# Optimization experiments

Measured on AMD Instinct MI355X. Metric: run time of the kernel, lower is better.

The kernel has to match this reference:

```python
import jax, jax.numpy as jnp
import numpy as np

B = 32        # events per batch
NP = 1024     # hits per event (in_hits)
K = 30        # kNN neighbors (includes self, as in PyG knn)
D_IN = 7      # hit feature dim (hardcoded SegmentationNet(7, ...))
OUT = 2       # out_channels


def _edge_conv(x, W1, b1, s, t, W2, b2, k):
    """DynamicEdgeConv: x [B,n,d] -> [B,n,64].
    kNN in feature space, edge MLP on [x_i, x_j - x_i], max-aggregate.
    BN (eval mode) folded into per-channel scale s and shift t."""
    sq = jnp.sum(x * x, axis=-1)                           # [B,n]
    d2 = sq[:, :, None] + sq[:, None, :] - 2.0 * jnp.einsum('bnd,bmd->bnm', x, x)
    _, idx = jax.lax.top_k(-d2, k)                         # [B,n,k] nearest (self included)
    xj = jax.vmap(lambda xb, ib: xb[ib])(x, idx)           # [B,n,k,d] gather neighbors
    xi = jnp.broadcast_to(x[:, :, None, :], xj.shape)
    e = jnp.concatenate([xi, xj - xi], axis=-1)            # [B,n,k,2d]
    h = jax.nn.relu((e @ W1 + b1) * s + t)                 # Linear + BN(eval) + ReLU
    h = h @ W2 + b2                                        # plain last layer (PyG MLP)
    return jnp.max(h, axis=2)                              # max aggregation over k


def setup_inputs() -> dict:
    key = jax.random.key(0)
    ks = jax.random.split(key, 40)
    def lin(k, fi, fo):
        return jax.random.normal(k, (fi, fo), jnp.float32) / np.float32(np.sqrt(fi))
    def vec(k, n, scale=0.1):
        return jax.random.normal(k, (n,), jnp.float32) * np.float32(scale)
    inp = {}
    inp['pos'] = jax.random.normal(ks[0], (B * NP, D_IN), jnp.float32)
    inp['batch'] = jnp.repeat(jnp.arange(B, dtype=jnp.int32), NP)
    inp['batch_size'] = B
    # conv1 edge MLP: [14,64] + BN + ReLU, [64,64]
    inp['c1_W1'] = lin(ks[1], 2 * D_IN, 64); inp['c1_b1'] = vec(ks[2], 64)
    inp['c1_s'] = 1.0 + vec(ks[3], 64); inp['c1_t'] = vec(ks[4], 64)
    inp['c1_W2'] = lin(ks[5], 64, 64); inp['c1_b2'] = vec(ks[6], 64)
    # conv2/conv3: [128,64] + BN + ReLU, [64,64]
    inp['c2_W1'] = lin(ks[7], 128, 64); inp['c2_b1'] = vec(ks[8], 64)
    inp['c2_s'] = 1.0 + vec(ks[9], 64); inp['c2_t'] = vec(ks[10], 64)
    inp['c2_W2'] = lin(ks[11], 64, 64); inp['c2_b2'] = vec(ks[12], 64)
    inp['c3_W1'] = lin(ks[13], 128, 64); inp['c3_b1'] = vec(ks[14], 64)
    inp['c3_s'] = 1.0 + vec(ks[15], 64); inp['c3_t'] = vec(ks[16], 64)
    inp['c3_W2'] = lin(ks[17], 64, 64); inp['c3_b2'] = vec(ks[18], 64)
    # segmentation head MLP [192,1024,256,128,OUT], norm=None, eval (dropout off)
    inp['h_W1'] = lin(ks[19], 192, 1024); inp['h_b1'] = vec(ks[20], 1024)
    inp['h_W2'] = lin(ks[21], 1024, 256); inp['h_b2'] = vec(ks[22], 256)
    inp['h_W3'] = lin(ks[23], 256, 128); inp['h_b3'] = vec(ks[24], 128)
    inp['h_W4'] = lin(ks[25], 128, OUT); inp['h_b4'] = vec(ks[26], OUT)
    # wrapper MLP: Linear(NP*OUT, 100), ReLU, Linear(100, OUT)
    inp['m_W1'] = lin(ks[27], NP * OUT, 100); inp['m_b1'] = vec(ks[28], 100)
    inp['m_W2'] = lin(ks[29], 100, OUT); inp['m_b2'] = vec(ks[30], OUT)
    return inp


def reference(pos, batch, batch_size,
              c1_W1, c1_b1, c1_s, c1_t, c1_W2, c1_b2,
              c2_W1, c2_b1, c2_s, c2_t, c2_W2, c2_b2,
              c3_W1, c3_b1, c3_s, c3_t, c3_W2, c3_b2,
              h_W1, h_b1, h_W2, h_b2, h_W3, h_b3, h_W4, h_b4,
              m_W1, m_b1, m_W2, m_b2):
    n = pos.shape[0] // batch_size
    x = pos.reshape(batch_size, n, -1)          # uniform contiguous graphs per `batch`
    x1 = _edge_conv(x, c1_W1, c1_b1, c1_s, c1_t, c1_W2, c1_b2, K)
    x2 = _edge_conv(x1, c2_W1, c2_b1, c2_s, c2_t, c2_W2, c2_b2, K)
    x3 = _edge_conv(x2, c3_W1, c3_b1, c3_s, c3_t, c3_W2, c3_b2, K)
    h = jnp.concatenate([x1, x2, x3], axis=-1)  # [B,n,192]
    h = jax.nn.relu(h @ h_W1 + h_b1)
    h = jax.nn.relu(h @ h_W2 + h_b2)
    h = jax.nn.relu(h @ h_W3 + h_b3)
    h = h @ h_W4 + h_b4
    seg = jax.nn.log_softmax(h, axis=-1)        # per-node log-probs [B,n,OUT]
    flat = seg.reshape(batch_size, -1)          # [B, n*OUT]
    y = jax.nn.relu(flat @ m_W1 + m_b1) @ m_W2 + m_b2
    return jax.nn.log_softmax(y, axis=-1)       # [B, OUT]
```

## Files before the change

kernel.cpp:

```cpp
#include <hip/hip_runtime.h>
#include <math.h>

#define NPB   1024
#define NB    32
#define NTOT  (NPB * NB)
#define KNN_K 30
#define QB    16
#define DSTR  1028
#define FINF  __builtin_inff()

typedef __attribute__((ext_vector_type(8))) short bf16x8;
typedef __attribute__((ext_vector_type(4))) float f32x4;
typedef unsigned short ushort_t;

__device__ inline ushort_t f2bf(float f) {
  unsigned u = __builtin_bit_cast(unsigned, f);
  u += 0x7FFFu + ((u >> 16) & 1u);
  return (ushort_t)(u >> 16);
}
__device__ inline float bf2f(ushort_t h) {
  return __builtin_bit_cast(float, (unsigned)h << 16);
}
__device__ inline unsigned packkey(float d, int col) {
  unsigned u = __builtin_bit_cast(unsigned, d);
  u ^= ((unsigned)((int)u >> 31) | 0x80000000u);
  return (u & 0xFFFFFC00u) | (unsigned)col;
}

__device__ __forceinline__ void select_row_packed(const unsigned* row, int jbase,
                                                  int* out, unsigned* cb, int lane) {
  unsigned u[16];
  #pragma unroll
  for (int i = 0; i < 16; ++i) u[i] = row[lane + (i << 6)];

  unsigned m = u[0];
  #pragma unroll
  for (int i = 1; i < 16; ++i) m = min(m, u[i]);
  #pragma unroll
  for (int k = 2; k <= 64; k <<= 1) {
    #pragma unroll
    for (int jj = k >> 1; jj >= 1; jj >>= 1) {
      const unsigned o = (unsigned)__shfl_xor((int)m, jj);
      const bool up    = ((lane & k) == 0);
      const bool lower = ((lane & jj) == 0);
      m = (lower == up) ? min(m, o) : max(m, o);
    }
  }
  const unsigned T = (unsigned)__shfl((int)m, 29);

  unsigned mask16 = 0; int cnt = 0;
  #pragma unroll
  for (int i = 0; i < 16; ++i) {
    const bool sv = (u[i] <= T);
    mask16 |= (sv ? 1u : 0u) << i;
    cnt += sv;
  }
  int sc = cnt;
  #pragma unroll
  for (int o = 1; o < 64; o <<= 1) {
    const int v = __shfl_up(sc, o);
    if (lane >= o) sc += v;
  }
  const int base = sc - cnt;
  const int tot  = __shfl(sc, 63);

  if (tot <= 128) {
    int p = base;
    #pragma unroll
    for (int i = 0; i < 16; ++i) {
      if ((mask16 >> i) & 1u) cb[p++] = u[i];
    }
    for (int q = tot + lane; q < 128; q += 64) cb[q] = 0xFFFFFFFFu;
    unsigned r0 = cb[lane];
    unsigned r1 = cb[lane + 64];
    #pragma unroll
    for (int k = 2; k <= 128; k <<= 1) {
      #pragma unroll
      for (int jj = k >> 1; jj >= 1; jj >>= 1) {
        if (jj == 64) {
          const unsigned lo = min(r0, r1), hi = max(r0, r1);
          r0 = lo; r1 = hi;
        } else {
          const unsigned o0 = (unsigned)__shfl_xor((int)r0, jj);
          const unsigned o1 = (unsigned)__shfl_xor((int)r1, jj);
          const bool lower = ((lane & jj) == 0);
          const bool up0 = ((lane & k) == 0);
          const bool up1 = (((lane + 64) & k) == 0);
          r0 = (lower == up0) ? min(r0, o0) : max(r0, o0);
          r1 = (lower == up1) ? min(r1, o1) : max(r1, o1);
        }
      }
    }
    if (lane < KNN_K) out[lane] = jbase + (int)(r0 & 1023u);
  } else {
    unsigned pk[16];
    #pragma unroll
    for (int i = 0; i < 16; ++i) pk[i] = u[i];
    #pragma unroll 1
    for (int k = 0; k < KNN_K; ++k) {
      unsigned best = pk[0];
      #pragma unroll
      for (int i = 1; i < 16; ++i) best = min(best, pk[i]);
      #pragma unroll
      for (int o = 32; o > 0; o >>= 1)
        best = min(best, (unsigned)__shfl_xor((int)best, o));
      if (lane == 0) out[k] = jbase + (int)(best & 1023u);
      #pragma unroll
      for (int i = 0; i < 16; ++i) if (pk[i] == best) pk[i] = 0xFFFFFFFFu;
    }
  }
}

__global__ __launch_bounds__(512)
void knn64_kernel(const ushort_t* __restrict__ X, int lda,
                  const float* __restrict__ sq, int* __restrict__ idx) {
  __shared__ unsigned d2l[QB * DSTR];
  __shared__ float sqa[QB];
  __shared__ unsigned cbuf[8][128];
  const int tid = threadIdx.x;
  const int wave = tid >> 6, lane = tid & 63;
  const int g = lane >> 4, r16 = lane & 15;
  const int nbase = blockIdx.y * NPB;
  const int q0 = blockIdx.x * QB;
  if (tid < QB) sqa[tid] = sq[nbase + q0 + tid];
  __syncthreads();

  const int n0 = wave * 128;
  bf16x8 a0[2];
  #pragma unroll
  for (int ks = 0; ks < 2; ++ks)
    a0[ks] = *(const bf16x8*)(X + (size_t)(nbase + q0 + r16) * lda + ks * 32 + g * 8);

  #pragma unroll
  for (int nt = 0; nt < 8; ++nt) {
    const int col = n0 + nt * 16 + r16;
    f32x4 acc0 = (f32x4)(0.f);
    #pragma unroll
    for (int ks = 0; ks < 2; ++ks) {
      const bf16x8 b = *(const bf16x8*)(X + (size_t)(nbase + col) * lda + ks * 32 + g * 8);
      acc0 = __builtin_amdgcn_mfma_f32_16x16x32_bf16(a0[ks], b, acc0, 0, 0, 0);
    }
    const float sb = sq[nbase + col];
    #pragma unroll
    for (int r = 0; r < 4; ++r) {
      const int row0 = g * 4 + r;
      d2l[row0 * DSTR + col] = packkey(sqa[row0] + sb - 2.f * acc0[r], col);
    }
  }
  __syncthreads();

  #pragma unroll 1
  for (int rr = 0; rr < 2; ++rr) {
    const int row = wave * 2 + rr;
    select_row_packed(&d2l[row * DSTR], nbase,
                      idx + (size_t)(nbase + q0 + row) * KNN_K, cbuf[wave], lane);
  }
}

__global__ __launch_bounds__(512)
void knn7_kernel(const float* __restrict__ pos,
                 const float* __restrict__ sq, int* __restrict__ idx) {
  __shared__ unsigned d2l[QB * DSTR];
  __shared__ float Xq[QB][8];
  __shared__ float sqa[QB];
  __shared__ unsigned cbuf[8][128];
  const int tid = threadIdx.x;
  const int wave = tid >> 6, lane = tid & 63;
  const int nbase = blockIdx.y * NPB;
  const int q0 = blockIdx.x * QB;
  if (tid < QB * 8) {
    const int row = tid >> 3, d = tid & 7;
    Xq[row][d] = (d < 7) ? pos[(size_t)(nbase + q0 + row) * 7 + d] : 0.f;
  }
  if (tid >= 256 && tid < 256 + QB) sqa[tid - 256] = sq[nbase + q0 + tid - 256];
  __syncthreads();

  const int c0 = wave * 128 + lane;
  float xc0[7], xc1[7];
  #pragma unroll
  for (int d = 0; d < 7; ++d) {
    xc0[d] = pos[(size_t)(nbase + c0) * 7 + d];
    xc1[d] = pos[(size_t)(nbase + c0 + 64) * 7 + d];
  }
  const float sb0 = sq[nbase + c0], sb1 = sq[nbase + c0 + 64];
  #pragma unroll 1
  for (int row = 0; row < QB; ++row) {
    float q[7];
    #pragma unroll
    for (int d = 0; d < 7; ++d) q[d] = Xq[row][d];
    float d0 = 0.f, d1 = 0.f;
    #pragma unroll
    for (int d = 0; d < 7; ++d) { d0 += q[d] * xc0[d]; d1 += q[d] * xc1[d]; }
    const float sa = sqa[row];
    d2l[row * DSTR + c0]      = packkey(sa + sb0 - 2.f * d0, c0);
    d2l[row * DSTR + c0 + 64] = packkey(sa + sb1 - 2.f * d1, c0 + 64);
  }
  __syncthreads();

  #pragma unroll 1
  for (int rr = 0; rr < 2; ++rr) {
    const int row = wave * 2 + rr;
    select_row_packed(&d2l[row * DSTR], nbase,
                      idx + (size_t)(nbase + q0 + row) * KNN_K, cbuf[wave], lane);
  }
}

template<int D>
__global__ __launch_bounds__(256)
void sq_kernel(const float* __restrict__ x, int lda, float* __restrict__ sq) {
  const int wave = threadIdx.x >> 6, c = threadIdx.x & 63;
  const int nb = blockIdx.x * 16 + wave * 4;
  #pragma unroll
  for (int i = 0; i < 4; ++i) {
    const float xv = (c < D) ? x[(size_t)(nb + i) * lda + c] : 0.f;
    float p = xv * xv;
    #pragma unroll
    for (int o = 32; o > 0; o >>= 1) p += __shfl_down(p, o);
    if (c == 0) sq[nb + i] = p;
  }
}
__global__ __launch_bounds__(256)
void sqbf_kernel(const ushort_t* __restrict__ x, int lda, float* __restrict__ sq) {
  const int wave = threadIdx.x >> 6, c = threadIdx.x & 63;
  const int nb = blockIdx.x * 16 + wave * 4;
  #pragma unroll
  for (int i = 0; i < 4; ++i) {
    const float xv = bf2f(x[(size_t)(nb + i) * lda + c]);
    float p = xv * xv;
    #pragma unroll
    for (int o = 32; o > 0; o >>= 1) p += __shfl_down(p, o);
    if (c == 0) sq[nb + i] = p;
  }
}

__global__ __launch_bounds__(256)
void wprep_kernel(const float* __restrict__ W1, const float* __restrict__ b1,
                  const float* __restrict__ s, const float* __restrict__ t,
                  int D, ushort_t* __restrict__ BTc, float* __restrict__ biasc) {
  const int i = blockIdx.x * 256 + threadIdx.x;
  if (i >= 128 * 64) return;
  const int n = i >> 6, k = i & 63;
  float v = 0.f;
  if (k < D) {
    if (n < 64) v = (W1[k * 64 + n] - W1[(D + k) * 64 + n]) * s[n];
    else        v = W1[(D + k) * 64 + (n - 64)] * s[n - 64];
  }
  BTc[i] = f2bf(v);
  if (k == 0) biasc[n] = (n < 64) ? (b1[n] * s[n] + t[n]) : 0.f;
}

__global__ __launch_bounds__(256)
void pospad_kernel(const float* __restrict__ pos, ushort_t* __restrict__ xpad) {
  const int i = blockIdx.x * 256 + threadIdx.x;
  const int node = i >> 6, k = i & 63;
  xpad[i] = f2bf(k < 7 ? pos[(size_t)node * 7 + k] : 0.f);
}

__global__ __launch_bounds__(256)
void wcvt_kernel(const float* __restrict__ W, ushort_t* __restrict__ BT,
                 int K, int N) {
  const int i = blockIdx.x * 256 + threadIdx.x;
  if (i >= N * K) return;
  const int n = i / K, k = i % K;
  BT[i] = f2bf(W[(size_t)k * N + n]);
}

__global__ __launch_bounds__(256)
void edge_mfma_kernel(const ushort_t* __restrict__ av,
                      const int* __restrict__ idx,
                      const ushort_t* __restrict__ W2T, const float* __restrict__ b2,
                      ushort_t* __restrict__ xbf) {
  const int lane = threadIdx.x & 63;
  const int wave = threadIdx.x >> 6;
  const int g = lane >> 4, r16 = lane & 15;
  const int node0 = blockIdx.x * 16 + wave * 4;

  bf16x8 bf[2][4];
  #pragma unroll
  for (int ks = 0; ks < 2; ++ks)
    #pragma unroll
    for (int nt = 0; nt < 4; ++nt)
      bf[ks][nt] = *(const bf16x8*)(W2T + (nt * 16 + r16) * 64 + ks * 32 + g * 8);

  const float b2c = b2[lane];

  #pragma unroll 1
  for (int nn = 0; nn < 4; ++nn) {
    const int node = node0 + nn;
    float asf[2][8];
    {
      const ushort_t* ar = av + (size_t)node * 128;
      #pragma unroll
      for (int ks = 0; ks < 2; ++ks) {
        union { uint4 v; ushort_t s[8]; } u;
        u.v = *(const uint4*)(ar + ks * 32 + g * 8);
        #pragma unroll
        for (int i = 0; i < 8; ++i) asf[ks][i] = bf2f(u.s[i]);
      }
    }
    const int j0 = idx[(size_t)node * KNN_K + r16];
    const int e1 = 16 + r16;
    const int j1 = idx[(size_t)node * KNN_K + (e1 < KNN_K ? e1 : KNN_K - 1)];

    f32x4 acc[2][4];
    #pragma unroll
    for (int mt = 0; mt < 2; ++mt)
      #pragma unroll
      for (int nt = 0; nt < 4; ++nt) acc[mt][nt] = (f32x4)(0.f);

    #pragma unroll
    for (int mt = 0; mt < 2; ++mt) {
      const int j = mt ? j1 : j0;
      const ushort_t* vr = av + (size_t)j * 128 + 64;
      #pragma unroll
      for (int ks = 0; ks < 2; ++ks) {
        union { uint4 v; ushort_t s[8]; } u;
        u.v = *(const uint4*)(vr + ks * 32 + g * 8);
        bf16x8 af;
        #pragma unroll
        for (int i = 0; i < 8; ++i) {
          const float hh = fmaxf(asf[ks][i] + bf2f(u.s[i]), 0.f);
          af[i] = (short)f2bf(hh);
        }
        #pragma unroll
        for (int nt = 0; nt < 4; ++nt)
          acc[mt][nt] = __builtin_amdgcn_mfma_f32_16x16x32_bf16(af, bf[ks][nt], acc[mt][nt], 0, 0, 0);
      }
    }

    float cm[4];
    #pragma unroll
    for (int nt = 0; nt < 4; ++nt) {
      float m0 = fmaxf(fmaxf(acc[0][nt][0], acc[0][nt][1]), fmaxf(acc[0][nt][2], acc[0][nt][3]));
      float m1 = fmaxf(fmaxf(acc[1][nt][0], acc[1][nt][1]), fmaxf(acc[1][nt][2], acc[1][nt][3]));
      float m = fmaxf(m0, m1);
      m = fmaxf(m, __shfl_xor(m, 16));
      m = fmaxf(m, __shfl_xor(m, 32));
      cm[nt] = m;
    }
    const float v = (g == 0) ? cm[0] : (g == 1) ? cm[1] : (g == 2) ? cm[2] : cm[3];
    xbf[(size_t)node * 192 + lane] = f2bf(v + b2c);
  }
}

template<bool RELU, typename CT>
__global__ __launch_bounds__(256)
void gemm_bf16_kernel(const ushort_t* __restrict__ A, int lda,
                      const ushort_t* __restrict__ BT, int ldb,
                      const float* __restrict__ bias,
                      CT* __restrict__ C, int ldc, int K) {
  __shared__ ushort_t As[128 * 72];
  __shared__ ushort_t Bs[128 * 72];
  const int tid = threadIdx.x;
  const int lane = tid & 63;
  const int g = lane >> 4, r16 = lane & 15;
  const int wv = tid >> 6, wm = wv >> 1, wn = wv & 1;
  const int bm = blockIdx.x * 128, bn = blockIdx.y * 128;

  f32x4 acc[4][4];
  #pragma unroll
  for (int mt = 0; mt < 4; ++mt)
    #pragma unroll
    for (int nt = 0; nt < 4; ++nt) acc[mt][nt] = (f32x4)(0.f);

  const int srow = tid >> 1, scq = (tid & 1) * 32;
  for (int k0 = 0; k0 < K; k0 += 64) {
    const ushort_t* ap = A + (size_t)(bm + srow) * lda + k0 + scq;
    const ushort_t* bp = BT + (size_t)(bn + srow) * ldb + k0 + scq;
    uint4 av0 = *(const uint4*)(ap);      uint4 av1 = *(const uint4*)(ap + 8);
    uint4 av2 = *(const uint4*)(ap + 16); uint4 av3 = *(const uint4*)(ap + 24);
    uint4 bv0 = *(const uint4*)(bp);      uint4 bv1 = *(const uint4*)(bp + 8);
    uint4 bv2 = *(const uint4*)(bp + 16); uint4 bv3 = *(const uint4*)(bp + 24);
    __syncthreads();
    *(uint4*)(As + srow * 72 + scq +  0) = av0;
    *(uint4*)(As + srow * 72 + scq +  8) = av1;
    *(uint4*)(As + srow * 72 + scq + 16) = av2;
    *(uint4*)(As + srow * 72 + scq + 24) = av3;
    *(uint4*)(Bs + srow * 72 + scq +  0) = bv0;
    *(uint4*)(Bs + srow * 72 + scq +  8) = bv1;
    *(uint4*)(Bs + srow * 72 + scq + 16) = bv2;
    *(uint4*)(Bs + srow * 72 + scq + 24) = bv3;
    __syncthreads();
    #pragma unroll
    for (int ks = 0; ks < 2; ++ks) {
      bf16x8 a[4], b[4];
      #pragma unroll
      for (int mt = 0; mt < 4; ++mt)
        a[mt] = *(const bf16x8*)(As + (wm * 64 + mt * 16 + r16) * 72 + ks * 32 + g * 8);
      #pragma unroll
      for (int nt = 0; nt < 4; ++nt)
        b[nt] = *(const bf16x8*)(Bs + (wn * 64 + nt * 16 + r16) * 72 + ks * 32 + g * 8);
      #pragma unroll
      for (int mt = 0; mt < 4; ++mt)
        #pragma unroll
        for (int nt = 0; nt < 4; ++nt)
          acc[mt][nt] = __builtin_amdgcn_mfma_f32_16x16x32_bf16(a[mt], b[nt], acc[mt][nt], 0, 0, 0);
    }
  }

  #pragma unroll
  for (int nt = 0; nt < 4; ++nt) {
    const int col = bn + wn * 64 + nt * 16 + r16;
    const float bv = bias[col];
    #pragma unroll
    for (int mt = 0; mt < 4; ++mt) {
      #pragma unroll
      for (int r = 0; r < 4; ++r) {
        const int row = bm + wm * 64 + mt * 16 + g * 4 + r;
        float val = acc[mt][nt][r] + bv;
        if (RELU) val = fmaxf(val, 0.f);
        if constexpr (sizeof(CT) == 2) C[(size_t)row * ldc + col] = f2bf(val);
        else                           C[(size_t)row * ldc + col] = val;
      }
    }
  }
}

__global__ __launch_bounds__(256)
void g4_kernel(const ushort_t* __restrict__ h3, const float* __restrict__ W4,
               const float* __restrict__ b4, float* __restrict__ seg) {
  const int row = blockIdx.x * 4 + (threadIdx.x >> 6);
  const int lane = threadIdx.x & 63;
  const ushort_t* hr = h3 + (size_t)row * 128;
  float p0 = 0.f, p1 = 0.f;
  #pragma unroll
  for (int h = 0; h < 2; ++h) {
    const int r = lane + h * 64;
    const float hv = bf2f(hr[r]);
    p0 += hv * W4[r * 2 + 0];
    p1 += hv * W4[r * 2 + 1];
  }
  #pragma unroll
  for (int o = 32; o > 0; o >>= 1) { p0 += __shfl_down(p0, o); p1 += __shfl_down(p1, o); }
  if (lane == 0) {
    const float l0 = p0 + b4[0], l1 = p1 + b4[1];
    const float mx = fmaxf(l0, l1);
    const float lse = mx + logf(expf(l0 - mx) + expf(l1 - mx));
    seg[(size_t)row * 2 + 0] = l0 - lse;
    seg[(size_t)row * 2 + 1] = l1 - lse;
  }
}

__global__ __launch_bounds__(256)
void wrapper_kernel(const float* __restrict__ seg, const float* __restrict__ W1,
                    const float* __restrict__ b1, const float* __restrict__ W2,
                    const float* __restrict__ b2, float* __restrict__ out) {
  __shared__ float fl[NPB * 2];
  __shared__ float part[2][128];
  __shared__ float y1[100];
  __shared__ float l2[2];
  const int b = blockIdx.x, tid = threadIdx.x;
  for (int i = tid; i < NPB * 2; i += 256) fl[i] = seg[(size_t)b * NPB * 2 + i];
  __syncthreads();
  {
    const int c = tid & 127, p = tid >> 7;
    float acc = 0.f;
    if (c < 100) {
      const int r0 = p * (NPB);
      #pragma unroll 16
      for (int r = 0; r < NPB; ++r)
        acc += fl[r0 + r] * W1[(size_t)(r0 + r) * 100 + c];
    }
    part[p][c] = acc;
  }
  __syncthreads();
  if (tid < 100) {
    y1[tid] = fmaxf(part[0][tid] + part[1][tid] + b1[tid], 0.f);
  }
  __syncthreads();
  if (tid < 2) {
    float acc = b2[tid];
    for (int j = 0; j < 100; ++j) acc += y1[j] * W2[j * 2 + tid];
    l2[tid] = acc;
  }
  __syncthreads();
  if (tid == 0) {
    const float l0 = l2[0], l1 = l2[1];
    const float mx = fmaxf(l0, l1);
    const float lse = mx + logf(expf(l0 - mx) + expf(l1 - mx));
    out[b * 2 + 0] = l0 - lse;
    out[b * 2 + 1] = l1 - lse;
  }
}

extern "C" void kernel_launch(void* const* d_in, const int* in_sizes, int n_in,
                              void* d_out, int out_size, void* d_ws, size_t ws_size,
                              hipStream_t stream) {
  const float* pos   = (const float*)d_in[0];
  const float* c1_W1 = (const float*)d_in[3];
  const float* c1_b1 = (const float*)d_in[4];
  const float* c1_s  = (const float*)d_in[5];
  const float* c1_t  = (const float*)d_in[6];
  const float* c1_W2 = (const float*)d_in[7];
  const float* c1_b2 = (const float*)d_in[8];
  const float* c2_W1 = (const float*)d_in[9];
  const float* c2_b1 = (const float*)d_in[10];
  const float* c2_s  = (const float*)d_in[11];
  const float* c2_t  = (const float*)d_in[12];
  const float* c2_W2 = (const float*)d_in[13];
  const float* c2_b2 = (const float*)d_in[14];
  const float* c3_W1 = (const float*)d_in[15];
  const float* c3_b1 = (const float*)d_in[16];
  const float* c3_s  = (const float*)d_in[17];
  const float* c3_t  = (const float*)d_in[18];
  const float* c3_W2 = (const float*)d_in[19];
  const float* c3_b2 = (const float*)d_in[20];
  const float* h_W1  = (const float*)d_in[21];
  const float* h_b1  = (const float*)d_in[22];
  const float* h_W2  = (const float*)d_in[23];
  const float* h_b2  = (const float*)d_in[24];
  const float* h_W3  = (const float*)d_in[25];
  const float* h_b3  = (const float*)d_in[26];
  const float* h_W4  = (const float*)d_in[27];
  const float* h_b4  = (const float*)d_in[28];
  const float* m_W1  = (const float*)d_in[29];
  const float* m_b1  = (const float*)d_in[30];
  const float* m_W2  = (const float*)d_in[31];
  const float* m_b2  = (const float*)d_in[32];

  float* ws = (float*)d_ws;
  size_t off = 0;
  auto alloc = [&](size_t n) {
    float* p = ws + off;
    off += (n + 63) & ~(size_t)63;
    return p;
  };
  ushort_t* xbf   = (ushort_t*)alloc((size_t)NTOT * 96);
  int*      idx   = (int*)alloc((size_t)NTOT * KNN_K);
  ushort_t* avbuf = (ushort_t*)alloc((size_t)NTOT * 64);
  ushort_t* xpad  = (ushort_t*)alloc((size_t)NTOT * 32);
  float*    sqb   = alloc(NTOT);
  float*    seg   = alloc((size_t)NTOT * 2);
  ushort_t* BT1   = (ushort_t*)alloc(1024 * 192 / 2);
  ushort_t* BT2   = (ushort_t*)alloc(256 * 1024 / 2);
  ushort_t* BT3   = (ushort_t*)alloc(128 * 256 / 2);
  ushort_t* BTc1  = (ushort_t*)alloc(128 * 64 / 2);
  ushort_t* BTc2  = (ushort_t*)alloc(128 * 64 / 2);
  ushort_t* BTc3  = (ushort_t*)alloc(128 * 64 / 2);
  ushort_t* W2T1  = (ushort_t*)alloc(64 * 64 / 2);
  ushort_t* W2T2  = (ushort_t*)alloc(64 * 64 / 2);
  ushort_t* W2T3  = (ushort_t*)alloc(64 * 64 / 2);
  float*    bc1   = alloc(128);
  float*    bc2   = alloc(128);
  float*    bc3   = alloc(128);

  const size_t totf = ws_size / 4;
  const size_t avail = (totf > off + 1024) ? (totf - off - 1024) : 0;
  int CH = 1;
  while (CH < 256 && (size_t)(NTOT / CH) * 704 > avail) CH <<= 1;
  const int CR = NTOT / CH;
  ushort_t* h1 = (ushort_t*)(ws + off);
  ushort_t* h2 = h1 + (size_t)CR * 1024;
  ushort_t* h3 = h2 + (size_t)CR * 256;

  wcvt_kernel<<<(192 * 1024 + 255) / 256, 256, 0, stream>>>(h_W1, BT1, 192, 1024);
  wcvt_kernel<<<(1024 * 256 + 255) / 256, 256, 0, stream>>>(h_W2, BT2, 1024, 256);
  wcvt_kernel<<<(256 * 128 + 255) / 256, 256, 0, stream>>>(h_W3, BT3, 256, 128);
  wcvt_kernel<<<16, 256, 0, stream>>>(c1_W2, W2T1, 64, 64);
  wcvt_kernel<<<16, 256, 0, stream>>>(c2_W2, W2T2, 64, 64);
  wcvt_kernel<<<16, 256, 0, stream>>>(c3_W2, W2T3, 64, 64);
  wprep_kernel<<<32, 256, 0, stream>>>(c1_W1, c1_b1, c1_s, c1_t, 7,  BTc1, bc1);
  wprep_kernel<<<32, 256, 0, stream>>>(c2_W1, c2_b1, c2_s, c2_t, 64, BTc2, bc2);
  wprep_kernel<<<32, 256, 0, stream>>>(c3_W1, c3_b1, c3_s, c3_t, 64, BTc3, bc3);
  pospad_kernel<<<NTOT * 64 / 256, 256, 0, stream>>>(pos, xpad);

  auto run_av = [&](const ushort_t* A, int lda, const ushort_t* BTc, const float* bc) {
    gemm_bf16_kernel<false, ushort_t><<<dim3(NTOT / 128, 1), 256, 0, stream>>>(
        A, lda, BTc, 64, bc, avbuf, 128, 64);
  };

  sq_kernel<7><<<NTOT / 16, 256, 0, stream>>>(pos, 7, sqb);
  run_av(xpad, 64, BTc1, bc1);
  knn7_kernel<<<dim3(NPB / QB, NB), 512, 0, stream>>>(pos, sqb, idx);
  edge_mfma_kernel<<<NTOT / 16, 256, 0, stream>>>(avbuf, idx, W2T1, c1_b2, xbf + 0);

  sqbf_kernel<<<NTOT / 16, 256, 0, stream>>>(xbf + 0, 192, sqb);
  run_av(xbf + 0, 192, BTc2, bc2);
  knn64_kernel<<<dim3(NPB / QB, NB), 512, 0, stream>>>(xbf + 0, 192, sqb, idx);
  edge_mfma_kernel<<<NTOT / 16, 256, 0, stream>>>(avbuf, idx, W2T2, c2_b2, xbf + 64);

  sqbf_kernel<<<NTOT / 16, 256, 0, stream>>>(xbf + 64, 192, sqb);
  run_av(xbf + 64, 192, BTc3, bc3);
  knn64_kernel<<<dim3(NPB / QB, NB), 512, 0, stream>>>(xbf + 64, 192, sqb, idx);
  edge_mfma_kernel<<<NTOT / 16, 256, 0, stream>>>(avbuf, idx, W2T3, c3_b2, xbf + 128);

  for (int ch = 0; ch < CH; ++ch) {
    const ushort_t* Ax = xbf + (size_t)ch * CR * 192;
    gemm_bf16_kernel<true, ushort_t><<<dim3(CR / 128, 8), 256, 0, stream>>>(Ax, 192, BT1, 192, h_b1, h1, 1024, 192);
    gemm_bf16_kernel<true, ushort_t><<<dim3(CR / 128, 2), 256, 0, stream>>>(h1, 1024, BT2, 1024, h_b2, h2, 256, 1024);
    gemm_bf16_kernel<true, ushort_t><<<dim3(CR / 128, 1), 256, 0, stream>>>(h2, 256, BT3, 256, h_b3, h3, 128, 256);
    g4_kernel<<<CR / 4, 256, 0, stream>>>(h3, h_W4, h_b4, seg + (size_t)ch * CR * 2);
  }

  wrapper_kernel<<<NB, 256, 0, stream>>>(seg, m_W1, m_b1, m_W2, m_b2, (float*)d_out);
}
```

Baseline: 414.1 us.

## Halve kNN query block, reuse distance row as candidate buffer, add 64-wide sort path

Cuts the kNN query block from 16 to 8 rows, so each wave selects one row and each block uses about half the LDS. That raises occupancy and doubles the block count. The separate candidate buffer is dropped, and the already-loaded distance row is reused in place to compact survivors. A new fast path handles up to 64 candidates with a single-register bitonic sort, skipping the 128-wide sort. In the MFMA path, half of the 16 rows computed are wasted and masked out, and the query-row loads are clamped.

```diff
diff --git a/kernel.cpp b/kernel.cpp
--- a/kernel.cpp
+++ b/kernel.cpp
@@ -5,7 +5,7 @@
 #define NB    32
 #define NTOT  (NPB * NB)
 #define KNN_K 30
-#define QB    16
+#define QB    8
 #define DSTR  1028
 #define FINF  __builtin_inff()
 
@@ -27,8 +27,8 @@
   return (u & 0xFFFFFC00u) | (unsigned)col;
 }
 
-__device__ __forceinline__ void select_row_packed(const unsigned* row, int jbase,
-                                                  int* out, unsigned* cb, int lane) {
+__device__ __forceinline__ void select_row_packed(unsigned* row, int jbase,
+                                                  int* out, int lane) {
   unsigned u[16];
   #pragma unroll
   for (int i = 0; i < 16; ++i) u[i] = row[lane + (i << 6)];
@@ -63,8 +63,28 @@
   }
   const int base = sc - cnt;
   const int tot  = __shfl(sc, 63);
-
-  if (tot <= 128) {
+  unsigned* cb = row;
+
+  if (tot <= 64) {
+    int p = base;
+    #pragma unroll
+    for (int i = 0; i < 16; ++i) {
+      if ((mask16 >> i) & 1u) cb[p++] = u[i];
+    }
+    if (tot + lane < 64) cb[tot + lane] = 0xFFFFFFFFu;
+    unsigned r0 = cb[lane];
+    #pragma unroll
+    for (int k = 2; k <= 64; k <<= 1) {
+      #pragma unroll
+      for (int jj = k >> 1; jj >= 1; jj >>= 1) {
+        const unsigned o = (unsigned)__shfl_xor((int)r0, jj);
+        const bool up    = ((lane & k) == 0);
+        const bool lower = ((lane & jj) == 0);
+        r0 = (lower == up) ? min(r0, o) : max(r0, o);
+      }
+    }
+    if (lane < KNN_K) out[lane] = jbase + (int)(r0 & 1023u);
+  } else if (tot <= 128) {
     int p = base;
     #pragma unroll
     for (int i = 0; i < 16; ++i) {
@@ -116,7 +136,6 @@
                   const float* __restrict__ sq, int* __restrict__ idx) {
   __shared__ unsigned d2l[QB * DSTR];
   __shared__ float sqa[QB];
-  __shared__ unsigned cbuf[8][128];
   const int tid = threadIdx.x;
   const int wave = tid >> 6, lane = tid & 63;
   const int g = lane >> 4, r16 = lane & 15;
@@ -126,10 +145,11 @@
   __syncthreads();
 
   const int n0 = wave * 128;
+  const int qr = (r16 < QB) ? r16 : QB - 1;
   bf16x8 a0[2];
   #pragma unroll
   for (int ks = 0; ks < 2; ++ks)
-    a0[ks] = *(const bf16x8*)(X + (size_t)(nbase + q0 + r16) * lda + ks * 32 + g * 8);
+    a0[ks] = *(const bf16x8*)(X + (size_t)(nbase + q0 + qr) * lda + ks * 32 + g * 8);
 
   #pragma unroll
   for (int nt = 0; nt < 8; ++nt) {
@@ -144,17 +164,15 @@
     #pragma unroll
     for (int r = 0; r < 4; ++r) {
       const int row0 = g * 4 + r;
-      d2l[row0 * DSTR + col] = packkey(sqa[row0] + sb - 2.f * acc0[r], col);
-    }
-  }
-  __syncthreads();
-
-  #pragma unroll 1
-  for (int rr = 0; rr < 2; ++rr) {
-    const int row = wave * 2 + rr;
-    select_row_packed(&d2l[row * DSTR], nbase,
-                      idx + (size_t)(nbase + q0 + row) * KNN_K, cbuf[wave], lane);
-  }
+      if (row0 < QB)
+        d2l[row0 * DSTR + col] = packkey(sqa[row0] + sb - 2.f * acc0[r], col);
+    }
+  }
+  __syncthreads();
+
+  const int row = wave;
+  select_row_packed(&d2l[row * DSTR], nbase,
+                    idx + (size_t)(nbase + q0 + row) * KNN_K, lane);
 }
 
 __global__ __launch_bounds__(512)
@@ -163,7 +181,6 @@
   __shared__ unsigned d2l[QB * DSTR];
   __shared__ float Xq[QB][8];
   __shared__ float sqa[QB];
-  __shared__ unsigned cbuf[8][128];
   const int tid = threadIdx.x;
   const int wave = tid >> 6, lane = tid & 63;
   const int nbase = blockIdx.y * NPB;
@@ -172,7 +189,7 @@
     const int row = tid >> 3, d = tid & 7;
     Xq[row][d] = (d < 7) ? pos[(size_t)(nbase + q0 + row) * 7 + d] : 0.f;
   }
-  if (tid >= 256 && tid < 256 + QB) sqa[tid - 256] = sq[nbase + q0 + tid - 256];
+  if (tid >= 64 && tid < 64 + QB) sqa[tid - 64] = sq[nbase + q0 + tid - 64];
   __syncthreads();
 
   const int c0 = wave * 128 + lane;
@@ -183,7 +200,7 @@
     xc1[d] = pos[(size_t)(nbase + c0 + 64) * 7 + d];
   }
   const float sb0 = sq[nbase + c0], sb1 = sq[nbase + c0 + 64];
-  #pragma unroll 1
+  #pragma unroll
   for (int row = 0; row < QB; ++row) {
     float q[7];
     #pragma unroll
@@ -197,12 +214,9 @@
   }
   __syncthreads();
 
-  #pragma unroll 1
-  for (int rr = 0; rr < 2; ++rr) {
-    const int row = wave * 2 + rr;
-    select_row_packed(&d2l[row * DSTR], nbase,
-                      idx + (size_t)(nbase + q0 + row) * KNN_K, cbuf[wave], lane);
-  }
+  const int row = wave;
+  select_row_packed(&d2l[row * DSTR], nbase,
+                    idx + (size_t)(nbase + q0 + row) * KNN_K, lane);
 }
 
 template<int D>
```

New measurement: 456.6 us. 1.1x slower.

## Replace bitonic kNN selection with ballot radix-select and fuse squared norms into edge kernel

Applied to the files above, without the earlier changes.

The per-row top-30 selection swaps the bitonic sorting networks (64-lane threshold sort and 128-element candidate sort) for a bitwise radix select built on ballot/popcount. Candidates are compacted into the distance row itself, which removes the separate cbuf shared buffer. When at most 64 candidates survive, they are written out in compacted order instead of fully sorted. The squared-norm computation for layers 2 and 3 moves into the edge_mfma epilogue, dropping two sqbf kernel launches and a reread of the features. The risks are a fixed 32-step ballot loop per select, and sq now being computed from the stored bf16 values inside the edge kernel rather than read back separately.

```diff
diff --git a/kernel.cpp b/kernel.cpp
--- a/kernel.cpp
+++ b/kernel.cpp
@@ -12,6 +12,7 @@
 typedef __attribute__((ext_vector_type(8))) short bf16x8;
 typedef __attribute__((ext_vector_type(4))) float f32x4;
 typedef unsigned short ushort_t;
+typedef unsigned long long ull_t;
 
 __device__ inline ushort_t f2bf(float f) {
   unsigned u = __builtin_bit_cast(unsigned, f);
@@ -27,8 +28,27 @@
   return (u & 0xFFFFFC00u) | (unsigned)col;
 }
 
-__device__ __forceinline__ void select_row_packed(const unsigned* row, int jbase,
-                                                  int* out, unsigned* cb, int lane) {
+__device__ __forceinline__ unsigned rank_val(unsigned v, int rank) {
+  ull_t act = ~0ull;
+  unsigned pre = 0;
+  int need = rank;
+  #pragma unroll
+  for (int bit = 31; bit >= 0; --bit) {
+    const ull_t zb = __ballot(((v >> bit) & 1u) == 0u) & act;
+    const int nz = __popcll(zb);
+    if (nz >= need) {
+      act = zb;
+    } else {
+      act &= ~zb;
+      need -= nz;
+      pre |= 1u << bit;
+    }
+  }
+  return pre;
+}
+
+__device__ __forceinline__ void select_row_packed(unsigned* row, int jbase,
+                                                  int* out, int lane) {
   unsigned u[16];
   #pragma unroll
   for (int i = 0; i < 16; ++i) u[i] = row[lane + (i << 6)];
@@ -36,62 +56,31 @@
   unsigned m = u[0];
   #pragma unroll
   for (int i = 1; i < 16; ++i) m = min(m, u[i]);
-  #pragma unroll
-  for (int k = 2; k <= 64; k <<= 1) {
-    #pragma unroll
-    for (int jj = k >> 1; jj >= 1; jj >>= 1) {
-      const unsigned o = (unsigned)__shfl_xor((int)m, jj);
-      const bool up    = ((lane & k) == 0);
-      const bool lower = ((lane & jj) == 0);
-      m = (lower == up) ? min(m, o) : max(m, o);
-    }
-  }
-  const unsigned T = (unsigned)__shfl((int)m, 29);
-
-  unsigned mask16 = 0; int cnt = 0;
+  const unsigned T1 = rank_val(m, KNN_K);
+
+  unsigned mask16 = 0;
+  #pragma unroll
+  for (int i = 0; i < 16; ++i)
+    mask16 |= ((u[i] <= T1) ? 1u : 0u) << i;
+
+  const ull_t ltm = (1ull << lane) - 1ull;
+  unsigned* cb = row;
+  int base = 0;
   #pragma unroll
   for (int i = 0; i < 16; ++i) {
-    const bool sv = (u[i] <= T);
-    mask16 |= (sv ? 1u : 0u) << i;
-    cnt += sv;
-  }
-  int sc = cnt;
-  #pragma unroll
-  for (int o = 1; o < 64; o <<= 1) {
-    const int v = __shfl_up(sc, o);
-    if (lane >= o) sc += v;
-  }
-  const int base = sc - cnt;
-  const int tot  = __shfl(sc, 63);
-
-  if (tot <= 128) {
-    int p = base;
-    #pragma unroll
-    for (int i = 0; i < 16; ++i) {
-      if ((mask16 >> i) & 1u) cb[p++] = u[i];
-    }
-    for (int q = tot + lane; q < 128; q += 64) cb[q] = 0xFFFFFFFFu;
-    unsigned r0 = cb[lane];
-    unsigned r1 = cb[lane + 64];
-    #pragma unroll
-    for (int k = 2; k <= 128; k <<= 1) {
-      #pragma unroll
-      for (int jj = k >> 1; jj >= 1; jj >>= 1) {
-        if (jj == 64) {
-          const unsigned lo = min(r0, r1), hi = max(r0, r1);
-          r0 = lo; r1 = hi;
-        } else {
-          const unsigned o0 = (unsigned)__shfl_xor((int)r0, jj);
-          const unsigned o1 = (unsigned)__shfl_xor((int)r1, jj);
-          const bool lower = ((lane & jj) == 0);
-          const bool up0 = ((lane & k) == 0);
-          const bool up1 = (((lane + 64) & k) == 0);
-          r0 = (lower == up0) ? min(r0, o0) : max(r0, o0);
-          r1 = (lower == up1) ? min(r1, o1) : max(r1, o1);
-        }
-      }
-    }
-    if (lane < KNN_K) out[lane] = jbase + (int)(r0 & 1023u);
+    const ull_t bm = __ballot((mask16 >> i) & 1u);
+    if ((mask16 >> i) & 1u)
+      cb[base + (int)__popcll(bm & ltm)] = u[i];
+    base += (int)__popcll(bm);
+  }
+  const int tot = base;
+
+  if (tot <= 64) {
+    const unsigned s = (lane < tot) ? cb[lane] : 0xFFFFFFFFu;
+    const unsigned T = rank_val(s, KNN_K);
+    const ull_t sel = __ballot(s <= T);
+    const int pos = (int)__popcll(sel & ltm);
+    if (s <= T) out[pos] = jbase + (int)(s & 1023u);
   } else {
     unsigned pk[16];
     #pragma unroll
@@ -116,7 +105,6 @@
                   const float* __restrict__ sq, int* __restrict__ idx) {
   __shared__ unsigned d2l[QB * DSTR];
   __shared__ float sqa[QB];
-  __shared__ unsigned cbuf[8][128];
   const int tid = threadIdx.x;
   const int wave = tid >> 6, lane = tid & 63;
   const int g = lane >> 4, r16 = lane & 15;
@@ -153,7 +141,7 @@
   for (int rr = 0; rr < 2; ++rr) {
     const int row = wave * 2 + rr;
     select_row_packed(&d2l[row * DSTR], nbase,
-                      idx + (size_t)(nbase + q0 + row) * KNN_K, cbuf[wave], lane);
+                      idx + (size_t)(nbase + q0 + row) * KNN_K, lane);
   }
 }
 
@@ -163,7 +151,6 @@
   __shared__ unsigned d2l[QB * DSTR];
   __shared__ float Xq[QB][8];
   __shared__ float sqa[QB];
-  __shared__ unsigned cbuf[8][128];
   const int tid = threadIdx.x;
   const int wave = tid >> 6, lane = tid & 63;
   const int nbase = blockIdx.y * NPB;
@@ -201,7 +188,7 @@
   for (int rr = 0; rr < 2; ++rr) {
     const int row = wave * 2 + rr;
     select_row_packed(&d2l[row * DSTR], nbase,
-                      idx + (size_t)(nbase + q0 + row) * KNN_K, cbuf[wave], lane);
+                      idx + (size_t)(nbase + q0 + row) * KNN_K, lane);
   }
 }
 
@@ -213,19 +200,6 @@
   #pragma unroll
   for (int i = 0; i < 4; ++i) {
     const float xv = (c < D) ? x[(size_t)(nb + i) * lda + c] : 0.f;
-    float p = xv * xv;
-    #pragma unroll
-    for (int o = 32; o > 0; o >>= 1) p += __shfl_down(p, o);
-    if (c == 0) sq[nb + i] = p;
-  }
-}
-__global__ __launch_bounds__(256)
-void sqbf_kernel(const ushort_t* __restrict__ x, int lda, float* __restrict__ sq) {
-  const int wave = threadIdx.x >> 6, c = threadIdx.x & 63;
-  const int nb = blockIdx.x * 16 + wave * 4;
-  #pragma unroll
-  for (int i = 0; i < 4; ++i) {
-    const float xv = bf2f(x[(size_t)(nb + i) * lda + c]);
     float p = xv * xv;
     #pragma unroll
     for (int o = 32; o > 0; o >>= 1) p += __shfl_down(p, o);
@@ -269,7 +243,7 @@
 void edge_mfma_kernel(const ushort_t* __restrict__ av,
                       const int* __restrict__ idx,
                       const ushort_t* __restrict__ W2T, const float* __restrict__ b2,
-                      ushort_t* __restrict__ xbf) {
+                      ushort_t* __restrict__ xbf, float* __restrict__ sqout) {
   const int lane = threadIdx.x & 63;
   const int wave = threadIdx.x >> 6;
   const int g = lane >> 4, r16 = lane & 15;
@@ -339,7 +313,13 @@
       cm[nt] = m;
     }
     const float v = (g == 0) ? cm[0] : (g == 1) ? cm[1] : (g == 2) ? cm[2] : cm[3];
-    xbf[(size_t)node * 192 + lane] = f2bf(v + b2c);
+    const ushort_t ob = f2bf(v + b2c);
+    xbf[(size_t)node * 192 + lane] = ob;
+    const float xv = bf2f(ob);
+    float p = xv * xv;
+    #pragma unroll
+    for (int o = 32; o > 0; o >>= 1) p += __shfl_down(p, o);
+    if (lane == 0) sqout[node] = p;
   }
 }
 
@@ -572,17 +552,15 @@
   sq_kernel<7><<<NTOT / 16, 256, 0, stream>>>(pos, 7, sqb);
   run_av(xpad, 64, BTc1, bc1);
   knn7_kernel<<<dim3(NPB / QB, NB), 512, 0, stream>>>(pos, sqb, idx);
-  edge_mfma_kernel<<<NTOT / 16, 256, 0, stream>>>(avbuf, idx, W2T1, c1_b2, xbf + 0);
-
-  sqbf_kernel<<<NTOT / 16, 256, 0, stream>>>(xbf + 0, 192, sqb);
+  edge_mfma_kernel<<<NTOT / 16, 256, 0, stream>>>(avbuf, idx, W2T1, c1_b2, xbf + 0, sqb);
+
   run_av(xbf + 0, 192, BTc2, bc2);
   knn64_kernel<<<dim3(NPB / QB, NB), 512, 0, stream>>>(xbf + 0, 192, sqb, idx);
-  edge_mfma_kernel<<<NTOT / 16, 256, 0, stream>>>(avbuf, idx, W2T2, c2_b2, xbf + 64);
-
-  sqbf_kernel<<<NTOT / 16, 256, 0, stream>>>(xbf + 64, 192, sqb);
+  edge_mfma_kernel<<<NTOT / 16, 256, 0, stream>>>(avbuf, idx, W2T2, c2_b2, xbf + 64, sqb);
+
   run_av(xbf + 64, 192, BTc3, bc3);
   knn64_kernel<<<dim3(NPB / QB, NB), 512, 0, stream>>>(xbf + 64, 192, sqb, idx);
-  edge_mfma_kernel<<<NTOT / 16, 256, 0, stream>>>(avbuf, idx, W2T3, c3_b2, xbf + 128);
+  edge_mfma_kernel<<<NTOT / 16, 256, 0, stream>>>(avbuf, idx, W2T3, c3_b2, xbf + 128, sqb);
 
   for (int ch = 0; ch < CH; ++ch) {
     const ushort_t* Ax = xbf + (size_t)ch * CR * 192;
```

Result: slower. 460.4 us (+11.2%).
